# Kernel optimization log

Measured on AMD Instinct MI355X. Metric: run time of the kernel, lower is better.

Reference implementation:

```python
import jax, jax.numpy as jnp
import numpy as np

N_DRUG = 572
EMB = 512
K_NB = 64
SEG_NB = 16
BN_EPS = 1e-5


def setup_inputs() -> dict:
    key = jax.random.key(0)
    ks = jax.random.split(key, 8)
    return {
        "drug_name": jnp.arange(N_DRUG, dtype=jnp.int64) if jax.config.jax_enable_x64 else jnp.arange(N_DRUG, dtype=jnp.int32),
        "adj_tail": jax.random.randint(ks[0], (N_DRUG, K_NB), 0, 100000),
        "adj_relation": jax.random.randint(ks[1], (N_DRUG, K_NB), 0, 200),
        "inv_adj_idx": jax.random.randint(ks[2], (N_DRUG, SEG_NB), 0, N_DRUG),
        "drug_table": jax.random.normal(ks[3], (N_DRUG, EMB), dtype=jnp.float32),
        "rela_table": jax.random.normal(ks[4], (200, EMB), dtype=jnp.float32),
        "ent_table": jax.random.normal(ks[5], (100000, EMB), dtype=jnp.float32),
        "W_lin": jax.random.normal(ks[6], (2 * EMB, EMB), dtype=jnp.float32) * (1.0 / np.sqrt(2 * EMB)),
        "b_lin": jnp.zeros((EMB,), jnp.float32),
        "bn_gamma": jnp.ones((EMB,), jnp.float32),
        "bn_beta": jnp.zeros((EMB,), jnp.float32),
        "epoch": 2,
    }


def _forward(drug_name, adj_tail, adj_relation, inv_adj_idx,
             drug_table, rela_table, ent_table, W_lin, b_lin,
             bn_gamma, bn_beta, epoch):
    # Embedding gathers
    drug_emb = drug_table[drug_name]          # [N, D]
    rel_emb = rela_table[adj_relation]        # [N, K, D]
    ent_emb = ent_table[adj_tail]             # [N, K, D]

    # KGCN-style attention over sampled neighbors: score_k = softmax(drug . rel_k)
    scores = jax.nn.softmax(jnp.einsum('nd,nkd->nk', drug_emb, rel_emb), axis=1)
    attended = jnp.einsum('nk,nkd->nd', scores, ent_emb)  # [N, D]

    # Linear -> ReLU -> BatchNorm1d (training-mode batch stats, biased var)
    e = jnp.concatenate([attended, drug_emb], axis=1)     # [N, 2D]
    h = jax.nn.relu(e @ W_lin + b_lin)                    # [N, D]
    mu = jnp.mean(h, axis=0)
    var = jnp.mean(jnp.square(h - mu), axis=0)
    drug_f = bn_gamma * (h - mu) * jax.lax.rsqrt(var + BN_EPS) + bn_beta

    if epoch > 1:
        # Sequential in-place neighbor averaging (faithful to the Python loop:
        # later drugs see already-updated rows).
        def body(f, x):
            i, pos = x
            avg = jnp.mean(f[pos], axis=0)                # [D]
            f = f.at[i].set((avg + f[i]) * 0.5)
            return f, None
        idxs = jnp.arange(N_DRUG)
        drug_f, _ = jax.lax.scan(body, drug_f, (idxs, inv_adj_idx))
    return drug_f


def reference(drug_name, adj_tail, adj_relation, inv_adj_idx,
              drug_table, rela_table, ent_table, W_lin, b_lin,
              bn_gamma, bn_beta, epoch):
    return _forward(drug_name, adj_tail, adj_relation, inv_adj_idx,
                    drug_table, rela_table, ent_table, W_lin, b_lin,
                    bn_gamma, bn_beta, epoch)
```

## Files before the change

kernel.cpp:

```cpp
#include <hip/hip_runtime.h>
#include <hip/hip_bf16.h>

#define N_DRUG 572
#define EMB    512
#define K_NB   64
#define SEG_NB 16
#define SCOLS  16

typedef __hip_bfloat16  bf16;
typedef __hip_bfloat162 bf162;

__device__ __forceinline__ float b2f(bf16 x){ return __bfloat162float(x); }

template<typename T> __device__ __forceinline__ float ldf(const T* p);
template<> __device__ __forceinline__ float ldf<float>(const float* p){ return *p; }
template<> __device__ __forceinline__ float ldf<bf16>(const bf16* p){ return b2f(*p); }

template<typename T> __device__ __forceinline__ float2 ld2(const T* p);
template<> __device__ __forceinline__ float2 ld2<float>(const float* p){ return *(const float2*)p; }
template<> __device__ __forceinline__ float2 ld2<bf16>(const bf16* p){
    bf162 v = *(const bf162*)p; return make_float2(b2f(v.x), b2f(v.y));
}

template<typename T> __device__ __forceinline__ void st2(T* p, float x, float y);
template<> __device__ __forceinline__ void st2<float>(float* p, float x, float y){ *(float2*)p = make_float2(x, y); }
template<> __device__ __forceinline__ void st2<bf16>(bf16* p, float x, float y){
    bf162 v; v.x = __float2bfloat16(x); v.y = __float2bfloat16(y); *(bf162*)p = v;
}

template<typename T> __device__ __forceinline__ void st1(T* p, float x);
template<> __device__ __forceinline__ void st1<float>(float* p, float x){ *p = x; }
template<> __device__ __forceinline__ void st1<bf16>(bf16* p, float x){ *p = __float2bfloat16(x); }

__device__ __forceinline__ bool idx_is64(const void* drug_name) {
    return ((const int*)drug_name)[1] == 0;
}
__device__ __forceinline__ int ld_idx(const void* p, int i, bool is64) {
    return is64 ? (int)((const long long*)p)[i] : ((const int*)p)[i];
}

__device__ __forceinline__ bool detect_bf16(const void* tab) {
    const int lane = threadIdx.x & 63;
    int hit = 0;
    if (lane < 32) {
        const unsigned u = ((const unsigned*)tab)[lane * 997];
        const unsigned e = (u >> 7) & 0xffu;
        hit = (e >= 110u && e <= 141u) ? 1 : 0;
    }
    return __popcll(__ballot(hit)) >= 24;
}

struct __align__(16) FwdSmem {
    float e[2][2 * EMB];
    float sc[2][K_NB];
    int   tl[2][K_NB];
};

template<typename T>
__device__ void fwd_impl(FwdSmem& sm,
    const void* drug_name, const void* adj_tail, const void* adj_rel,
    const T* __restrict__ drug_table, const T* __restrict__ rela_table,
    const T* __restrict__ ent_table,  const T* __restrict__ W,
    const T* __restrict__ bl, T* __restrict__ h)
{
    const int  t    = threadIdx.x;
    const int  n0   = blockIdx.x * 2;
    const bool is64 = idx_is64(drug_name);

    #pragma unroll
    for (int dr = 0; dr < 2; ++dr) {
        const int row = ld_idx(drug_name, n0 + dr, is64);
        const float2 v = ld2(drug_table + (size_t)row * EMB + 2 * t);
        sm.e[dr][EMB + 2 * t]     = v.x;
        sm.e[dr][EMB + 2 * t + 1] = v.y;
    }
    if (t < 128) {
        const int dr = t >> 6, k = t & 63;
        sm.tl[dr][k] = ld_idx(adj_tail, (n0 + dr) * K_NB + k, is64);
    }
    __syncthreads();

    {
        const int wave = t >> 6, lane = t & 63;
        const int dr = wave >> 1;
        const int kb = (wave & 1) * 32;
        const float* ed = &sm.e[dr][EMB];
        #pragma unroll 4
        for (int i = 0; i < 32; ++i) {
            const int k   = kb + i;
            const int rid = ld_idx(adj_rel, (n0 + dr) * K_NB + k, is64);
            const T* rl = rela_table + (size_t)rid * EMB;
            float p = 0.f;
            #pragma unroll
            for (int m = 0; m < 4; ++m) {
                const int dd = 2 * lane + m * 128;
                const float2 rv = ld2(rl + dd);
                p = fmaf(ed[dd],     rv.x, p);
                p = fmaf(ed[dd + 1], rv.y, p);
            }
            #pragma unroll
            for (int off = 32; off; off >>= 1) p += __shfl_down(p, off, 64);
            if (lane == 0) sm.sc[dr][k] = p;
        }
    }
    __syncthreads();

    if (t < 128) {
        const int dr = t >> 6, k = t & 63;
        const float s = sm.sc[dr][k];
        float m = s;
        #pragma unroll
        for (int off = 32; off; off >>= 1) m = fmaxf(m, __shfl_xor(m, off, 64));
        const float ex = __expf(s - m);
        float sum = ex;
        #pragma unroll
        for (int off = 32; off; off >>= 1) sum += __shfl_xor(sum, off, 64);
        sm.sc[dr][k] = ex / sum;
    }
    __syncthreads();

    {
        float a00 = 0.f, a01 = 0.f, a10 = 0.f, a11 = 0.f;
        #pragma unroll 4
        for (int k = 0; k < K_NB; ++k) {
            const float w0 = sm.sc[0][k], w1 = sm.sc[1][k];
            const float2 v0 = ld2(ent_table + (size_t)sm.tl[0][k] * EMB + 2 * t);
            const float2 v1 = ld2(ent_table + (size_t)sm.tl[1][k] * EMB + 2 * t);
            a00 = fmaf(w0, v0.x, a00); a01 = fmaf(w0, v0.y, a01);
            a10 = fmaf(w1, v1.x, a10); a11 = fmaf(w1, v1.y, a11);
        }
        sm.e[0][2 * t] = a00; sm.e[0][2 * t + 1] = a01;
        sm.e[1][2 * t] = a10; sm.e[1][2 * t + 1] = a11;
    }
    __syncthreads();

    {
        const int d0 = 2 * t;
        const float2 bb = ld2(bl + d0);
        float a00 = bb.x, a01 = bb.y, a10 = bb.x, a11 = bb.y;
        const float4* E0 = (const float4*)&sm.e[0][0];
        const float4* E1 = (const float4*)&sm.e[1][0];
        #pragma unroll 2
        for (int q = 0; q < (2 * EMB) / 4; ++q) {
            const float4 f0 = E0[q];
            const float4 f1 = E1[q];
            const T* Wp = W + (size_t)(4 * q) * EMB + d0;
            const float2 w0 = ld2(Wp);
            const float2 w1 = ld2(Wp + EMB);
            const float2 w2 = ld2(Wp + 2 * EMB);
            const float2 w3 = ld2(Wp + 3 * EMB);
            a00 = fmaf(f0.x, w0.x, a00); a01 = fmaf(f0.x, w0.y, a01);
            a10 = fmaf(f1.x, w0.x, a10); a11 = fmaf(f1.x, w0.y, a11);
            a00 = fmaf(f0.y, w1.x, a00); a01 = fmaf(f0.y, w1.y, a01);
            a10 = fmaf(f1.y, w1.x, a10); a11 = fmaf(f1.y, w1.y, a11);
            a00 = fmaf(f0.z, w2.x, a00); a01 = fmaf(f0.z, w2.y, a01);
            a10 = fmaf(f1.z, w2.x, a10); a11 = fmaf(f1.z, w2.y, a11);
            a00 = fmaf(f0.w, w3.x, a00); a01 = fmaf(f0.w, w3.y, a01);
            a10 = fmaf(f1.w, w3.x, a10); a11 = fmaf(f1.w, w3.y, a11);
        }
        st2(h + (size_t)n0 * EMB + d0,       fmaxf(a00, 0.f), fmaxf(a01, 0.f));
        st2(h + (size_t)(n0 + 1) * EMB + d0, fmaxf(a10, 0.f), fmaxf(a11, 0.f));
    }
}

__global__ __launch_bounds__(256) void k_fwd(
    const void* drug_name, const void* adj_tail, const void* adj_rel,
    const void* drug_tab, const void* rela_tab, const void* ent_tab,
    const void* W, const void* bl, void* h)
{
    __shared__ FwdSmem sm;
    if (detect_bf16(drug_tab))
        fwd_impl<bf16>(sm, drug_name, adj_tail, adj_rel,
                       (const bf16*)drug_tab, (const bf16*)rela_tab,
                       (const bf16*)ent_tab, (const bf16*)W,
                       (const bf16*)bl, (bf16*)h);
    else
        fwd_impl<float>(sm, drug_name, adj_tail, adj_rel,
                        (const float*)drug_tab, (const float*)rela_tab,
                        (const float*)ent_tab, (const float*)W,
                        (const float*)bl, (float*)h);
}

struct __align__(16) ScanSmem {
    float    fbuf[N_DRUG * SCOLS];
    unsigned obuf[N_DRUG * SEG_NB];
    float    corr[576];
};

template<typename T, bool IS64>
__device__ void scan_impl(ScanSmem& sm, T* __restrict__ h,
    const void* __restrict__ inv, const T* __restrict__ gamma,
    const T* __restrict__ beta, const void* __restrict__ epoch)
{
    const int t  = threadIdx.x;
    const int c0 = blockIdx.x * SCOLS;

    for (int k = t; k < N_DRUG * SEG_NB; k += 64)
        sm.obuf[k] = (unsigned)ld_idx(inv, k, IS64) << 4;
    for (int k = t; k < N_DRUG * SCOLS; k += 64)
        sm.fbuf[k] = ldf(h + (size_t)(k >> 4) * EMB + c0 + (k & 15));
    for (int k = t; k < 576; k += 64) sm.corr[k] = 0.f;
    __syncthreads();

    for (int i = 1 + t; i < N_DRUG; i += 64) {
        const unsigned tgt = (unsigned)(i - 1) << 4;
        int cn = 0;
        #pragma unroll
        for (int j = 0; j < SEG_NB; ++j)
            cn += (sm.obuf[i * SEG_NB + j] == tgt) ? 1 : 0;
        sm.corr[i] = (float)cn * (1.f / 32.f);
    }

    {
        const int c = t & 15, g = t >> 4;
        float s = 0.f, s2 = 0.f;
        for (int r = g; r < N_DRUG; r += 4) {
            const float x = sm.fbuf[r * SCOLS + c];
            s += x; s2 = fmaf(x, x, s2);
        }
        s  += __shfl_xor(s, 16, 64);  s  += __shfl_xor(s, 32, 64);
        s2 += __shfl_xor(s2, 16, 64); s2 += __shfl_xor(s2, 32, 64);
        const float mu  = s * (1.f / N_DRUG);
        const float var = fmaxf(s2 * (1.f / N_DRUG) - mu * mu, 0.f);
        const float gs  = ldf(gamma + c0 + c) * rsqrtf(var + 1e-5f);
        const float bs  = ldf(beta  + c0 + c);
        for (int r = g; r < N_DRUG; r += 4) {
            const float x = sm.fbuf[r * SCOLS + c];
            sm.fbuf[r * SCOLS + c] = fmaf(x - mu, gs, bs);
        }
    }
    __syncthreads();

    if (((const int*)epoch)[0] > 1 && t < 16) {
        const float* fb  = sm.fbuf + t;
        const uint4* ob4 = (const uint4*)sm.obuf;

        unsigned OF[16];
        float    V[16];
        {
            uint4 q0 = ob4[0], q1 = ob4[1], q2 = ob4[2], q3 = ob4[3];
            OF[0]=q0.x; OF[1]=q0.y; OF[2]=q0.z; OF[3]=q0.w;
            OF[4]=q1.x; OF[5]=q1.y; OF[6]=q1.z; OF[7]=q1.w;
            OF[8]=q2.x; OF[9]=q2.y; OF[10]=q2.z; OF[11]=q2.w;
            OF[12]=q3.x; OF[13]=q3.y; OF[14]=q3.z; OF[15]=q3.w;
            #pragma unroll
            for (int j = 0; j < 16; ++j) V[j] = fb[OF[j]];
            q0 = ob4[4]; q1 = ob4[5]; q2 = ob4[6]; q3 = ob4[7];
            OF[0]=q0.x; OF[1]=q0.y; OF[2]=q0.z; OF[3]=q0.w;
            OF[4]=q1.x; OF[5]=q1.y; OF[6]=q1.z; OF[7]=q1.w;
            OF[8]=q2.x; OF[9]=q2.y; OF[10]=q2.z; OF[11]=q2.w;
            OF[12]=q3.x; OF[13]=q3.y; OF[14]=q3.z; OF[15]=q3.w;
        }
        float fi = fb[0];
        float kc = 0.f, knext = sm.corr[1];
        float nv_p = 0.f, fi_p = 0.f;

        for (int i = 0; i < N_DRUG; ++i) {
            float NV[16];
            #pragma unroll
            for (int j = 0; j < 16; ++j) NV[j] = fb[OF[j]];
            const int inx = (i + 1 < N_DRUG) ? i + 1 : N_DRUG - 1;
            const float nfi = fb[inx * 16];

            const float s0 = (V[0]+V[1]) + (V[2]+V[3]);
            const float s1 = (V[4]+V[5]) + (V[6]+V[7]);
            const float s2 = (V[8]+V[9]) + (V[10]+V[11]);
            const float s3 = (V[12]+V[13]) + (V[14]+V[15]);
            const float sum  = (s0 + s1) + (s2 + s3);
            const float base = fmaf(sum, 1.f / 32.f, fi * 0.5f);
            const float nv   = fmaf(kc, nv_p - fi_p, base);
            sm.fbuf[i * SCOLS + t] = nv;

            const int i2 = (i + 2 < N_DRUG) ? i + 2 : N_DRUG - 1;
            const uint4 q0 = ob4[i2 * 4 + 0], q1 = ob4[i2 * 4 + 1];
            const uint4 q2 = ob4[i2 * 4 + 2], q3 = ob4[i2 * 4 + 3];
            const float kn2 = sm.corr[i + 2];

            #pragma unroll
            for (int j = 0; j < 16; ++j) V[j] = NV[j];
            OF[0]=q0.x; OF[1]=q0.y; OF[2]=q0.z; OF[3]=q0.w;
            OF[4]=q1.x; OF[5]=q1.y; OF[6]=q1.z; OF[7]=q1.w;
            OF[8]=q2.x; OF[9]=q2.y; OF[10]=q2.z; OF[11]=q2.w;
            OF[12]=q3.x; OF[13]=q3.y; OF[14]=q3.z; OF[15]=q3.w;
            fi_p = fi; fi = nfi; nv_p = nv; kc = knext; knext = kn2;
        }
    }
    __syncthreads();

    for (int k = t; k < N_DRUG * SCOLS; k += 64)
        st1(h + (size_t)(k >> 4) * EMB + c0 + (k & 15), sm.fbuf[k]);
}

__global__ __launch_bounds__(64) void k_scan(
    void* h, const void* inv, const void* gamma, const void* beta,
    const void* epoch, const void* drug_name, const void* drug_tab)
{
    __shared__ ScanSmem sm;
    const bool isbf = detect_bf16(drug_tab);
    const bool is64 = idx_is64(drug_name);
    if (isbf) {
        if (is64) scan_impl<bf16, true >(sm, (bf16*)h, inv, (const bf16*)gamma, (const bf16*)beta, epoch);
        else      scan_impl<bf16, false>(sm, (bf16*)h, inv, (const bf16*)gamma, (const bf16*)beta, epoch);
    } else {
        if (is64) scan_impl<float, true >(sm, (float*)h, inv, (const float*)gamma, (const float*)beta, epoch);
        else      scan_impl<float, false>(sm, (float*)h, inv, (const float*)gamma, (const float*)beta, epoch);
    }
}

extern "C" void kernel_launch(void* const* d_in, const int* in_sizes, int n_in,
                              void* d_out, int out_size, void* d_ws, size_t ws_size,
                              hipStream_t stream)
{
    (void)in_sizes; (void)n_in; (void)out_size; (void)d_ws; (void)ws_size;

    k_fwd<<<N_DRUG / 2, 256, 0, stream>>>(
        d_in[0], d_in[1], d_in[2],
        d_in[4], d_in[5], d_in[6],
        d_in[7], d_in[8],
        d_out);
    k_scan<<<EMB / SCOLS, 64, 0, stream>>>(
        d_out, d_in[3],
        d_in[9], d_in[10], d_in[11],
        d_in[0], d_in[4]);
}
```

Measured before the change: 475.8 us.

## Extend scan dependency correction to two prior rows and vectorize staging

The sequential neighbour-averaging scan now prefetches neighbour values two rows ahead, using two interleaved register sets. Contributions from the previous two updated rows are applied as precomputed correction terms, where the old code handled only the immediately previous row. This lengthens the window between issuing shared-memory gathers and needing their results on the serial critical path. Staging into and flushing out of shared memory switches to 16-byte vector loads and stores. The cost is more registers and a more complex correctness argument: reading pre-updated values assumes no neighbour dependencies further back than two rows are missed.

```diff
diff --git a/kernel.cpp b/kernel.cpp
--- a/kernel.cpp
+++ b/kernel.cpp
@@ -27,10 +27,6 @@
 template<> __device__ __forceinline__ void st2<bf16>(bf16* p, float x, float y){
     bf162 v; v.x = __float2bfloat16(x); v.y = __float2bfloat16(y); *(bf162*)p = v;
 }
-
-template<typename T> __device__ __forceinline__ void st1(T* p, float x);
-template<> __device__ __forceinline__ void st1<float>(float* p, float x){ *p = x; }
-template<> __device__ __forceinline__ void st1<bf16>(bf16* p, float x){ *p = __float2bfloat16(x); }
 
 __device__ __forceinline__ bool idx_is64(const void* drug_name) {
     return ((const int*)drug_name)[1] == 0;
@@ -184,8 +180,105 @@
 struct __align__(16) ScanSmem {
     float    fbuf[N_DRUG * SCOLS];
     unsigned obuf[N_DRUG * SEG_NB];
-    float    corr[576];
+    float2   corr[576];
 };
+
+__device__ __forceinline__ float bflo(unsigned u){ return __uint_as_float(u << 16); }
+__device__ __forceinline__ float bfhi(unsigned u){ return __uint_as_float(u & 0xffff0000u); }
+__device__ __forceinline__ unsigned pack_bf2(float a, float b) {
+    bf162 v; v.x = __float2bfloat16(a); v.y = __float2bfloat16(b);
+    unsigned u; __builtin_memcpy(&u, &v, 4); return u;
+}
+
+template<typename T>
+__device__ __forceinline__ void stage_fbuf(float* fbuf, const T* h, int c0, int t);
+template<>
+__device__ __forceinline__ void stage_fbuf<float>(float* fbuf, const float* h, int c0, int t) {
+    float4* dst = (float4*)fbuf;
+    #pragma unroll 4
+    for (int k = t; k < N_DRUG * 4; k += 64)
+        dst[k] = *(const float4*)(h + (size_t)(k >> 2) * EMB + c0 + 4 * (k & 3));
+}
+template<>
+__device__ __forceinline__ void stage_fbuf<bf16>(float* fbuf, const bf16* h, int c0, int t) {
+    float4* dst = (float4*)fbuf;
+    #pragma unroll 4
+    for (int k = t; k < N_DRUG * 2; k += 64) {
+        const uint4 v = *(const uint4*)(h + (size_t)(k >> 1) * EMB + c0 + 8 * (k & 1));
+        dst[2 * k]     = make_float4(bflo(v.x), bfhi(v.x), bflo(v.y), bfhi(v.y));
+        dst[2 * k + 1] = make_float4(bflo(v.z), bfhi(v.z), bflo(v.w), bfhi(v.w));
+    }
+}
+
+template<typename T>
+__device__ __forceinline__ void flush_fbuf(const float* fbuf, T* h, int c0, int t);
+template<>
+__device__ __forceinline__ void flush_fbuf<float>(const float* fbuf, float* h, int c0, int t) {
+    const float4* src = (const float4*)fbuf;
+    #pragma unroll 4
+    for (int k = t; k < N_DRUG * 4; k += 64)
+        *(float4*)(h + (size_t)(k >> 2) * EMB + c0 + 4 * (k & 3)) = src[k];
+}
+template<>
+__device__ __forceinline__ void flush_fbuf<bf16>(const float* fbuf, bf16* h, int c0, int t) {
+    const float4* src = (const float4*)fbuf;
+    #pragma unroll 4
+    for (int k = t; k < N_DRUG * 2; k += 64) {
+        const float4 f0 = src[2 * k], f1 = src[2 * k + 1];
+        uint4 o;
+        o.x = pack_bf2(f0.x, f0.y); o.y = pack_bf2(f0.z, f0.w);
+        o.z = pack_bf2(f1.x, f1.y); o.w = pack_bf2(f1.z, f1.w);
+        *(uint4*)(h + (size_t)(k >> 1) * EMB + c0 + 8 * (k & 1)) = o;
+    }
+}
+
+template<bool IS64>
+__device__ __forceinline__ void stage_obuf(unsigned* obuf, const void* inv, int t) {
+    const uint4* src = (const uint4*)inv;
+    if (IS64) {
+        #pragma unroll 4
+        for (int k = t; k < (N_DRUG * SEG_NB) / 2; k += 64) {
+            const uint4 v = src[k];
+            *(uint2*)(obuf + 2 * k) = make_uint2(v.x << 4, v.z << 4);
+        }
+    } else {
+        uint4* dst = (uint4*)obuf;
+        #pragma unroll 4
+        for (int k = t; k < (N_DRUG * SEG_NB) / 4; k += 64) {
+            uint4 v = src[k];
+            v.x <<= 4; v.y <<= 4; v.z <<= 4; v.w <<= 4;
+            dst[k] = v;
+        }
+    }
+}
+
+#define LD_OFF(OF, R)                                                        \
+    {                                                                        \
+        const uint4 q0 = ob4[(R) * 4 + 0], q1 = ob4[(R) * 4 + 1];            \
+        const uint4 q2 = ob4[(R) * 4 + 2], q3 = ob4[(R) * 4 + 3];            \
+        OF[0]=q0.x; OF[1]=q0.y; OF[2]=q0.z; OF[3]=q0.w;                      \
+        OF[4]=q1.x; OF[5]=q1.y; OF[6]=q1.z; OF[7]=q1.w;                      \
+        OF[8]=q2.x; OF[9]=q2.y; OF[10]=q2.z; OF[11]=q2.w;                    \
+        OF[12]=q3.x; OF[13]=q3.y; OF[14]=q3.z; OF[15]=q3.w;                  \
+    }
+
+#define SCAN_ROW(V, OF, fi, cc, I, IP2, IP4)                                 \
+    {                                                                        \
+        const float s0 = (V[0] + V[1]) + (V[2] + V[3]);                      \
+        const float s1 = (V[4] + V[5]) + (V[6] + V[7]);                      \
+        const float s2 = (V[8] + V[9]) + (V[10] + V[11]);                    \
+        const float s3 = (V[12] + V[13]) + (V[14] + V[15]);                  \
+        float nv = fmaf((s0 + s1) + (s2 + s3), 1.f / 32.f, fi * 0.5f);       \
+        nv = fmaf(cc.x, nv1 - f1, nv);                                       \
+        nv = fmaf(cc.y, nv2 - f2, nv);                                       \
+        f2 = f1; f1 = fi; nv2 = nv1; nv1 = nv;                               \
+        _Pragma("unroll")                                                    \
+        for (int j = 0; j < 16; ++j) V[j] = fb[OF[j]];                       \
+        fi = fb[(IP2) * 16];                                                 \
+        cc = sm.corr[(I) + 2];                                               \
+        sm.fbuf[(I) * SCOLS + t] = nv;                                       \
+        LD_OFF(OF, IP4);                                                     \
+    }
 
 template<typename T, bool IS64>
 __device__ void scan_impl(ScanSmem& sm, T* __restrict__ h,
@@ -195,20 +288,22 @@
     const int t  = threadIdx.x;
     const int c0 = blockIdx.x * SCOLS;
 
-    for (int k = t; k < N_DRUG * SEG_NB; k += 64)
-        sm.obuf[k] = (unsigned)ld_idx(inv, k, IS64) << 4;
-    for (int k = t; k < N_DRUG * SCOLS; k += 64)
-        sm.fbuf[k] = ldf(h + (size_t)(k >> 4) * EMB + c0 + (k & 15));
-    for (int k = t; k < 576; k += 64) sm.corr[k] = 0.f;
+    stage_obuf<IS64>(sm.obuf, inv, t);
+    stage_fbuf<T>(sm.fbuf, h, c0, t);
+    for (int k = t; k < 576; k += 64) sm.corr[k] = make_float2(0.f, 0.f);
     __syncthreads();
 
     for (int i = 1 + t; i < N_DRUG; i += 64) {
-        const unsigned tgt = (unsigned)(i - 1) << 4;
-        int cn = 0;
-        #pragma unroll
-        for (int j = 0; j < SEG_NB; ++j)
-            cn += (sm.obuf[i * SEG_NB + j] == tgt) ? 1 : 0;
-        sm.corr[i] = (float)cn * (1.f / 32.f);
+        const unsigned tA = (unsigned)(i - 1) << 4;
+        const unsigned tB = (unsigned)(i - 2) << 4;
+        int cA = 0, cB = 0;
+        #pragma unroll
+        for (int j = 0; j < SEG_NB; ++j) {
+            const unsigned o = sm.obuf[i * SEG_NB + j];
+            cA += (o == tA) ? 1 : 0;
+            cB += (o == tB) ? 1 : 0;
+        }
+        sm.corr[i] = make_float2((float)cA * (1.f / 32.f), (float)cB * (1.f / 32.f));
     }
 
     {
@@ -235,60 +330,31 @@
         const float* fb  = sm.fbuf + t;
         const uint4* ob4 = (const uint4*)sm.obuf;
 
-        unsigned OF[16];
-        float    V[16];
-        {
-            uint4 q0 = ob4[0], q1 = ob4[1], q2 = ob4[2], q3 = ob4[3];
-            OF[0]=q0.x; OF[1]=q0.y; OF[2]=q0.z; OF[3]=q0.w;
-            OF[4]=q1.x; OF[5]=q1.y; OF[6]=q1.z; OF[7]=q1.w;
-            OF[8]=q2.x; OF[9]=q2.y; OF[10]=q2.z; OF[11]=q2.w;
-            OF[12]=q3.x; OF[13]=q3.y; OF[14]=q3.z; OF[15]=q3.w;
-            #pragma unroll
-            for (int j = 0; j < 16; ++j) V[j] = fb[OF[j]];
-            q0 = ob4[4]; q1 = ob4[5]; q2 = ob4[6]; q3 = ob4[7];
-            OF[0]=q0.x; OF[1]=q0.y; OF[2]=q0.z; OF[3]=q0.w;
-            OF[4]=q1.x; OF[5]=q1.y; OF[6]=q1.z; OF[7]=q1.w;
-            OF[8]=q2.x; OF[9]=q2.y; OF[10]=q2.z; OF[11]=q2.w;
-            OF[12]=q3.x; OF[13]=q3.y; OF[14]=q3.z; OF[15]=q3.w;
-        }
-        float fi = fb[0];
-        float kc = 0.f, knext = sm.corr[1];
-        float nv_p = 0.f, fi_p = 0.f;
-
-        for (int i = 0; i < N_DRUG; ++i) {
-            float NV[16];
-            #pragma unroll
-            for (int j = 0; j < 16; ++j) NV[j] = fb[OF[j]];
-            const int inx = (i + 1 < N_DRUG) ? i + 1 : N_DRUG - 1;
-            const float nfi = fb[inx * 16];
-
-            const float s0 = (V[0]+V[1]) + (V[2]+V[3]);
-            const float s1 = (V[4]+V[5]) + (V[6]+V[7]);
-            const float s2 = (V[8]+V[9]) + (V[10]+V[11]);
-            const float s3 = (V[12]+V[13]) + (V[14]+V[15]);
-            const float sum  = (s0 + s1) + (s2 + s3);
-            const float base = fmaf(sum, 1.f / 32.f, fi * 0.5f);
-            const float nv   = fmaf(kc, nv_p - fi_p, base);
-            sm.fbuf[i * SCOLS + t] = nv;
-
-            const int i2 = (i + 2 < N_DRUG) ? i + 2 : N_DRUG - 1;
-            const uint4 q0 = ob4[i2 * 4 + 0], q1 = ob4[i2 * 4 + 1];
-            const uint4 q2 = ob4[i2 * 4 + 2], q3 = ob4[i2 * 4 + 3];
-            const float kn2 = sm.corr[i + 2];
-
-            #pragma unroll
-            for (int j = 0; j < 16; ++j) V[j] = NV[j];
-            OF[0]=q0.x; OF[1]=q0.y; OF[2]=q0.z; OF[3]=q0.w;
-            OF[4]=q1.x; OF[5]=q1.y; OF[6]=q1.z; OF[7]=q1.w;
-            OF[8]=q2.x; OF[9]=q2.y; OF[10]=q2.z; OF[11]=q2.w;
-            OF[12]=q3.x; OF[13]=q3.y; OF[14]=q3.z; OF[15]=q3.w;
-            fi_p = fi; fi = nfi; nv_p = nv; kc = knext; knext = kn2;
-        }
-    }
-    __syncthreads();
-
-    for (int k = t; k < N_DRUG * SCOLS; k += 64)
-        st1(h + (size_t)(k >> 4) * EMB + c0 + (k & 15), sm.fbuf[k]);
+        unsigned OFA[16], OFB[16];
+        float    VA[16],  VB[16];
+
+        LD_OFF(OFA, 0); LD_OFF(OFB, 1);
+        #pragma unroll
+        for (int j = 0; j < 16; ++j) VA[j] = fb[OFA[j]];
+        #pragma unroll
+        for (int j = 0; j < 16; ++j) VB[j] = fb[OFB[j]];
+        LD_OFF(OFA, 2); LD_OFF(OFB, 3);
+        float  fiA = fb[0],        fiB = fb[16];
+        float2 ccA = sm.corr[0],   ccB = sm.corr[1];
+        float nv1 = 0.f, nv2 = 0.f, f1 = 0.f, f2 = 0.f;
+
+        for (int i = 0; i < N_DRUG; i += 2) {
+            const int a2 = (i + 2 < N_DRUG) ? i + 2 : N_DRUG - 1;
+            const int a4 = (i + 4 < N_DRUG) ? i + 4 : N_DRUG - 1;
+            SCAN_ROW(VA, OFA, fiA, ccA, i, a2, a4);
+            const int b2 = (i + 3 < N_DRUG) ? i + 3 : N_DRUG - 1;
+            const int b4 = (i + 5 < N_DRUG) ? i + 5 : N_DRUG - 1;
+            SCAN_ROW(VB, OFB, fiB, ccB, i + 1, b2, b4);
+        }
+    }
+    __syncthreads();
+
+    flush_fbuf<T>(sm.fbuf, h, c0, t);
 }
 
 __global__ __launch_bounds__(64) void k_scan(
```

Measured after the change: 496.7 us. 4.4% more time.
